# Kernel tuning notes

Measured on AMD Instinct MI355X. Metric: run time of the kernel, lower is better.

The kernel has to match this reference:

```python
import jax, jax.numpy as jnp
import numpy as np

NUM_NODES = 1024
INPUT_DIM = 64
HID_DIM = 64
MAX_DIFFUSION_STEP = 2
NUM_SUPPORTS = 2
OUT_DIM = 128
INPUT_SIZE = INPUT_DIM + HID_DIM          # F = 128
NUM_MATRICES = NUM_SUPPORTS * MAX_DIFFUSION_STEP + 1  # M = 5
BATCH = 64


def setup_inputs() -> dict:
    key = jax.random.key(0)
    k1, k2, k3, k4 = jax.random.split(key, 4)
    # scale supports like a normalized random-walk matrix so diffusion stays bounded
    supports = jax.random.normal(k1, (NUM_SUPPORTS, NUM_NODES, NUM_NODES), jnp.float32) / np.float32(np.sqrt(NUM_NODES))
    inputs = jax.random.normal(k2, (BATCH, NUM_NODES * INPUT_DIM), jnp.float32)
    state = jax.random.normal(k3, (BATCH, NUM_NODES * HID_DIM), jnp.float32)
    weight = jax.random.normal(k4, (INPUT_SIZE * NUM_MATRICES, OUT_DIM), jnp.float32) * 0.05
    biases = jnp.zeros((OUT_DIM,), jnp.float32)
    return {"supports": supports, "inputs": inputs, "state": state,
            "weight": weight, "biases": biases, "output_size": OUT_DIM}


def reference(supports, inputs, state, weight, biases, output_size):
    B = inputs.shape[0]
    x_in = inputs.reshape(B, NUM_NODES, -1)   # [B, N, input_dim]
    st = state.reshape(B, NUM_NODES, -1)      # [B, N, hid_dim]
    x0 = jnp.concatenate([x_in, st], axis=2)  # [B, N, F]

    xs = [x0]
    # Chebyshev-style diffusion: x_k = 2*A@x_{k-1} - x_{k-2}, per support
    for s in range(NUM_SUPPORTS):
        A = supports[s]
        x1 = jnp.einsum('nm,bmf->bnf', A, x0)
        xs.append(x1)
        xp2, xp1 = x0, x1
        for _ in range(2, MAX_DIFFUSION_STEP + 1):
            x2 = 2.0 * jnp.einsum('nm,bmf->bnf', A, xp1) - xp2
            xs.append(x2)
            xp2, xp1 = xp1, x2

    # torch does stack on dim1 -> [B,M,N,F], transpose to [B,N,F,M], reshape to F*M.
    # stacking on the last axis gives [B,N,F,M] directly (same memory order f*M+m).
    x = jnp.stack(xs, axis=3)                               # [B, N, F, M]
    x = x.reshape(B * NUM_NODES, INPUT_SIZE * NUM_MATRICES)  # [B*N, F*M]
    out = x @ weight + biases                                # [B*N, output_size]
    return out.reshape(B, NUM_NODES * output_size)
```

## Files before the change

### kernel.cpp

```cpp
#include <hip/hip_runtime.h>
#include <hip/hip_bf16.h>


typedef short bf16x8  __attribute__((ext_vector_type(8)));
typedef short short4v __attribute__((ext_vector_type(4)));
typedef float f32x4   __attribute__((ext_vector_type(4)));

constexpr size_t MB1    = 1024ull * 1024ull;
constexpr size_t SZ_MAT = 8192ull * 1024ull;
constexpr size_t OFF_PSTK = 0;
constexpr size_t OFF_SUPT = 4 * MB1;
constexpr size_t OFF_X0T  = 6 * MB1;
constexpr size_t OFF_X0NF = OFF_X0T  + SZ_MAT;
constexpr size_t OFF_XNF  = OFF_X0NF + SZ_MAT;
constexpr size_t OFF_W2T  = OFF_XNF  + 4 * SZ_MAT;

__device__ __forceinline__ unsigned short f2bf(float x) {
  union { float f; unsigned int u; } v; v.f = x;
  unsigned int r = v.u + 0x7fffu + ((v.u >> 16) & 1u);
  return (unsigned short)(r >> 16);
}

#define GLD16(gp, lp)                                                         \
  __builtin_amdgcn_global_load_lds(                                           \
      (const __attribute__((address_space(1))) unsigned int*)(gp),            \
      (__attribute__((address_space(3))) unsigned int*)(lp), 16, 0, 0)


__global__ __launch_bounds__(256)
void prep_kernel(const float* __restrict__ sup,
                 const float* __restrict__ weight,
                 const float* __restrict__ inputs,
                 const float* __restrict__ state,
                 unsigned short* __restrict__ ws) {
  __shared__ unsigned short tile[64][65];
  int bid = blockIdx.x;
  int tl  = threadIdx.x;

  if (bid < 2048) {
    size_t t = (size_t)bid * 256 + tl;
    const float4* src = (const float4*)sup;
    float4 v = src[t];
    size_t e = t * 4;
    size_t s = e >> 20;
    size_t r = e & (MB1 - 1);
    short4v o; o[0] = (short)f2bf(v.x); o[1] = (short)f2bf(v.y);
    o[2] = (short)f2bf(v.z); o[3] = (short)f2bf(v.w);
    *(short4v*)&ws[OFF_PSTK + 2 * s * MB1 + r] = o;
  } else if (bid < 2560) {
    int i = bid - 2048;
    int nt = i & 15, mt = (i >> 4) & 15, s = i >> 8;
    const float* A = sup + (size_t)s * MB1;
    unsigned short* AT = ws + OFF_SUPT + (size_t)s * MB1;
    int cl = tl & 63, rg = tl >> 6;
#pragma unroll 4
    for (int rr = 0; rr < 16; ++rr) {
      int rl = rr * 4 + rg;
      tile[rl][cl] = f2bf(A[(size_t)(nt * 64 + rl) * 1024 + mt * 64 + cl]);
    }
    __syncthreads();
#pragma unroll 4
    for (int rr = 0; rr < 16; ++rr) {
      int ml = rr * 4 + rg;
      AT[(size_t)(mt * 64 + ml) * 1024 + nt * 64 + cl] = tile[cl][ml];
    }
  } else if (bid < 2880) {
    int t = (bid - 2560) * 256 + tl;
    int o = t / 640, k = t % 640;
    int m = k >> 7, f = k & 127;
    ws[OFF_W2T + t] = f2bf(weight[(f * 5 + m) * 128 + o]);
  } else {
    int i = bid - 2880;
    int b = i & 63, nt = (i >> 6) & 15, ft = i >> 10;
    const float* src = ft ? state : inputs;
    unsigned short* x0t  = ws + OFF_X0T;
    unsigned short* x0nf = ws + OFF_X0NF;
    int fl = tl & 63, nr = tl >> 6;
#pragma unroll 4
    for (int rr = 0; rr < 16; ++rr) {
      int n_loc = rr * 4 + nr;
      float v = src[(size_t)b * 65536 + (size_t)(nt * 64 + n_loc) * 64 + fl];
      unsigned short bv = f2bf(v);
      tile[n_loc][fl] = bv;
      x0nf[(size_t)(nt * 64 + n_loc) * 8192 + b * 128 + ft * 64 + fl] = bv;
    }
    __syncthreads();
#pragma unroll 4
    for (int rr = 0; rr < 16; ++rr) {
      int f_loc = rr * 4 + nr;
      x0t[(size_t)(b * 128 + ft * 64 + f_loc) * 1024 + nt * 64 + fl] =
          tile[fl][f_loc];
    }
  }
}


__global__ __launch_bounds__(256, 2)
void mega_kernel(unsigned short* __restrict__ ws,
                 const float* __restrict__ bias,
                 float* __restrict__ dout) {
  extern __shared__ unsigned short lds[];

  const unsigned short* X0T = ws + OFF_X0T;
  const unsigned short* X0N = ws + OFF_X0NF;
  const unsigned short* W2  = ws + OFF_W2T;

  const int tid = threadIdx.x;
  const int l   = tid & 63;
  const int w   = tid >> 6;
  const int wr  = w >> 1, wc = w & 1;
  const int lm  = l & 15, q = l >> 4;

  int bid = blockIdx.x;
  int xcd = bid & 7, idx = bid >> 3;
  const int bm = xcd * 8 + (idx & 7);
  const int bn = idx >> 3;

  const int subrow = l >> 3;
  const int koff   = (((l & 7) << 3) ^ (subrow << 3));

  auto stage_x0t = [&](int kt) {
#pragma unroll
    for (int c = 0; c < 4; ++c) {
      int chunk = w * 4 + c, rowl = chunk * 8 + subrow;
      const unsigned short* gp =
          X0T + (size_t)(bm * 128 + rowl) * 1024 + kt * 64 + koff;
      GLD16(gp, &lds[chunk * 512]);
    }
  };
  auto stage_P = [&](int band, int kt) {
#pragma unroll
    for (int c = 0; c < 4; ++c) {
      int chunk = w * 4 + c, rowl = chunk * 8 + subrow;
      const unsigned short* gp = ws + OFF_PSTK + (size_t)band * MB1 +
                                 (size_t)(bn * 128 + rowl) * 1024 + kt * 64 + koff;
      GLD16(gp, &lds[8192 + chunk * 512]);
    }
  };
  auto stage_w2 = [&](int m, int kt2) {
#pragma unroll
    for (int c = 0; c < 4; ++c) {
      int chunk = w * 4 + c, rowl = chunk * 8 + subrow;
      const unsigned short* gp =
          W2 + (size_t)rowl * 640 + m * 128 + kt2 * 64 + koff;
      GLD16(gp, &lds[chunk * 512]);
    }
  };
  auto stage_x0n = [&](int kt2) {
#pragma unroll
    for (int c = 0; c < 4; ++c) {
      int chunk = w * 4 + c, rowl = chunk * 8 + subrow;
      const unsigned short* gp =
          X0N + (size_t)(bn * 128 + rowl) * 8192 + bm * 128 + kt2 * 64 + koff;
      GLD16(gp, &lds[8192 + chunk * 512]);
    }
  };

  f32x4 oacc[4][4] = {};

  for (int band = 0; band < 4; ++band) {
    f32x4 yacc[4][4] = {};
    for (int kt = 0; kt < 16; ++kt) {
      stage_x0t(kt);
      stage_P(band, kt);
      __syncthreads();
#pragma unroll
      for (int kk = 0; kk < 2; ++kk) {
        bf16x8 af[4], bfv[4];
#pragma unroll
        for (int i = 0; i < 4; ++i) {
          int row = wr * 64 + i * 16 + lm;
          int off = row * 64 + ((kk * 32 + (q << 3)) ^ ((row & 7) << 3));
          af[i] = *(const bf16x8*)&lds[off];
        }
#pragma unroll
        for (int j = 0; j < 4; ++j) {
          int row = wc * 64 + j * 16 + lm;
          int off = 8192 + row * 64 + ((kk * 32 + (q << 3)) ^ ((row & 7) << 3));
          bfv[j] = *(const bf16x8*)&lds[off];
        }
#pragma unroll
        for (int i = 0; i < 4; ++i)
#pragma unroll
          for (int j = 0; j < 4; ++j)
            yacc[i][j] = __builtin_amdgcn_mfma_f32_16x16x32_bf16(
                af[i], bfv[j], yacc[i][j], 0, 0, 0);
      }
      __syncthreads();
    }

#pragma unroll
    for (int i = 0; i < 4; ++i) {
      int f0 = wr * 64 + i * 16 + q * 4;
#pragma unroll
      for (int j = 0; j < 4; ++j) {
        int n = wc * 64 + j * 16 + lm;
        short4v pk;
#pragma unroll
        for (int r = 0; r < 4; ++r) pk[r] = (short)f2bf(yacc[i][j][r]);
        *(short4v*)&lds[16384 + n * 128 + (((f0 >> 3) ^ (n & 7)) << 3) +
                        (f0 & 7)] = pk;
      }
    }
    __syncthreads();

#pragma unroll
    for (int kt2 = 0; kt2 < 2; ++kt2) {
      stage_w2(band + 1, kt2);
      __syncthreads();
#pragma unroll
      for (int kk = 0; kk < 2; ++kk) {
        bf16x8 af[4], bfv[4];
#pragma unroll
        for (int i = 0; i < 4; ++i) {
          int row = wr * 64 + i * 16 + lm;
          int off = row * 64 + ((kk * 32 + (q << 3)) ^ ((row & 7) << 3));
          af[i] = *(const bf16x8*)&lds[off];
        }
#pragma unroll
        for (int j = 0; j < 4; ++j) {
          int n = wc * 64 + j * 16 + lm;
          int g = kt2 * 8 + kk * 4 + q;
          bfv[j] = *(const bf16x8*)&lds[16384 + n * 128 + ((g ^ (n & 7)) << 3)];
        }
#pragma unroll
        for (int i = 0; i < 4; ++i)
#pragma unroll
          for (int j = 0; j < 4; ++j)
            oacc[i][j] = __builtin_amdgcn_mfma_f32_16x16x32_bf16(
                af[i], bfv[j], oacc[i][j], 0, 0, 0);
      }
      __syncthreads();
    }
  }

#pragma unroll
  for (int kt2 = 0; kt2 < 2; ++kt2) {
    stage_w2(0, kt2);
    stage_x0n(kt2);
    __syncthreads();
#pragma unroll
    for (int kk = 0; kk < 2; ++kk) {
      bf16x8 af[4], bfv[4];
#pragma unroll
      for (int i = 0; i < 4; ++i) {
        int row = wr * 64 + i * 16 + lm;
        int off = row * 64 + ((kk * 32 + (q << 3)) ^ ((row & 7) << 3));
        af[i] = *(const bf16x8*)&lds[off];
      }
#pragma unroll
      for (int j = 0; j < 4; ++j) {
        int row = wc * 64 + j * 16 + lm;
        int off = 8192 + row * 64 + ((kk * 32 + (q << 3)) ^ ((row & 7) << 3));
        bfv[j] = *(const bf16x8*)&lds[off];
      }
#pragma unroll
      for (int i = 0; i < 4; ++i)
#pragma unroll
        for (int j = 0; j < 4; ++j)
          oacc[i][j] = __builtin_amdgcn_mfma_f32_16x16x32_bf16(
              af[i], bfv[j], oacc[i][j], 0, 0, 0);
    }
    __syncthreads();
  }

#pragma unroll
  for (int i = 0; i < 4; ++i) {
    int o0 = wr * 64 + i * 16 + q * 4;
    float4 bv = *(const float4*)&bias[o0];
#pragma unroll
    for (int j = 0; j < 4; ++j) {
      int n = bn * 128 + wc * 64 + j * 16 + lm;
      float4 v;
      v.x = oacc[i][j][0] + bv.x;
      v.y = oacc[i][j][1] + bv.y;
      v.z = oacc[i][j][2] + bv.z;
      v.w = oacc[i][j][3] + bv.w;
      *(float4*)&dout[(size_t)bm * 131072 + (size_t)n * 128 + o0] = v;
    }
  }
}


__global__ __launch_bounds__(256)
void psq_kernel(unsigned short* __restrict__ ws) {
  __shared__ short At[128 * 64];
  __shared__ short Bt[32 * 64];

  const int tid = threadIdx.x;
  const int l   = tid & 63;
  const int w   = tid >> 6;
  const int wr  = w >> 1, wc = w & 1;

  const int bm = blockIdx.x, bn = blockIdx.y, s = blockIdx.z;
  const unsigned short* A = ws + OFF_PSTK + (size_t)(2 * s) * MB1;
  const unsigned short* B = ws + OFF_SUPT + (size_t)s * MB1;

  const int subrow = l >> 3;
  const int koff   = (((l & 7) << 3) ^ (subrow << 3));

  f32x4 acc[4][1] = {};

  for (int kt = 0; kt < 16; ++kt) {
#pragma unroll
    for (int c = 0; c < 4; ++c) {
      int chunk = w * 4 + c, rowl = chunk * 8 + subrow;
      GLD16(A + (size_t)(bm * 128 + rowl) * 1024 + kt * 64 + koff,
            &At[chunk * 512]);
    }
    {
      int chunk = w, rowl = chunk * 8 + subrow;
      GLD16(B + (size_t)(bn * 32 + rowl) * 1024 + kt * 64 + koff,
            &Bt[chunk * 512]);
    }
    __syncthreads();

#pragma unroll
    for (int kk = 0; kk < 2; ++kk) {
      bf16x8 af[4], bfv;
#pragma unroll
      for (int i = 0; i < 4; ++i) {
        int row = wr * 64 + i * 16 + (l & 15);
        int off = row * 64 + ((kk * 32 + ((l >> 4) << 3)) ^ ((row & 7) << 3));
        af[i] = *(const bf16x8*)&At[off];
      }
      {
        int row = wc * 16 + (l & 15);
        int off = row * 64 + ((kk * 32 + ((l >> 4) << 3)) ^ ((row & 7) << 3));
        bfv = *(const bf16x8*)&Bt[off];
      }
#pragma unroll
      for (int i = 0; i < 4; ++i)
        acc[i][0] = __builtin_amdgcn_mfma_f32_16x16x32_bf16(af[i], bfv,
                                                            acc[i][0], 0, 0, 0);
    }
    __syncthreads();
  }

  unsigned short* P = ws + OFF_PSTK + (size_t)(2 * s + 1) * MB1;
#pragma unroll
  for (int i = 0; i < 4; ++i) {
    int rg0 = bm * 128 + wr * 64 + i * 16 + ((l >> 4) << 2);
    int cg  = bn * 32 + wc * 16 + (l & 15);
#pragma unroll
    for (int r = 0; r < 4; ++r) {
      int rg = rg0 + r;
      float v = 2.0f * acc[i][0][r] - (rg == cg ? 1.0f : 0.0f);
      P[(size_t)rg * 1024 + cg] = f2bf(v);
    }
  }
}


extern "C" void kernel_launch(void* const* d_in, const int* in_sizes, int n_in,
                              void* d_out, int out_size, void* d_ws, size_t ws_size,
                              hipStream_t stream) {
  (void)in_sizes; (void)n_in; (void)out_size; (void)ws_size;
  const float* supports = (const float*)d_in[0];
  const float* inputs   = (const float*)d_in[1];
  const float* state    = (const float*)d_in[2];
  const float* weight   = (const float*)d_in[3];
  const float* bias     = (const float*)d_in[4];
  float* out = (float*)d_out;
  unsigned short* ws = (unsigned short*)d_ws;

  prep_kernel<<<4928, 256, 0, stream>>>(supports, weight, inputs, state, ws);
  psq_kernel<<<dim3(8, 32, 2), 256, 0, stream>>>(ws);
  mega_kernel<<<512, 256, 65536, stream>>>(ws, bias, out);
}
```

Baseline: 113.7 us.

## Process two diffusion bands per K-loop to reuse X0T tiles across bands

The first GEMM now accumulates two P bands at once, with two P tiles staged in LDS per k-step. Each X0T tile is therefore loaded and read from LDS once for two bands, which halves the passes over X0T. The second GEMM now works in halves: only the half of the warps whose rows match writes its Y slice into a smaller LDS region before each W2 half-step. The cost is twice the yacc accumulator registers (a second 4x4 block per thread), a larger LDS footprint, and extra barriers.

Result: slower. 124.1 us (+9.2%).

```diff
diff --git a/kernel.cpp b/kernel.cpp
--- a/kernel.cpp
+++ b/kernel.cpp
@@ -128,21 +128,21 @@
       GLD16(gp, &lds[chunk * 512]);
     }
   };
-  auto stage_P = [&](int band, int kt) {
+  auto stage_P = [&](int band, int kt, int slot) {
 #pragma unroll
     for (int c = 0; c < 4; ++c) {
       int chunk = w * 4 + c, rowl = chunk * 8 + subrow;
       const unsigned short* gp = ws + OFF_PSTK + (size_t)band * MB1 +
                                  (size_t)(bn * 128 + rowl) * 1024 + kt * 64 + koff;
-      GLD16(gp, &lds[8192 + chunk * 512]);
+      GLD16(gp, &lds[8192 + slot * 8192 + chunk * 512]);
     }
   };
-  auto stage_w2 = [&](int m, int kt2) {
+  auto stage_w2 = [&](int m, int h) {
 #pragma unroll
     for (int c = 0; c < 4; ++c) {
       int chunk = w * 4 + c, rowl = chunk * 8 + subrow;
       const unsigned short* gp =
-          W2 + (size_t)rowl * 640 + m * 128 + kt2 * 64 + koff;
+          W2 + (size_t)rowl * 640 + m * 128 + h * 64 + koff;
       GLD16(gp, &lds[chunk * 512]);
     }
   };
@@ -158,15 +158,16 @@
 
   f32x4 oacc[4][4] = {};
 
-  for (int band = 0; band < 4; ++band) {
-    f32x4 yacc[4][4] = {};
+  for (int s = 0; s < 2; ++s) {
+    f32x4 yacc[2][4][4] = {};
     for (int kt = 0; kt < 16; ++kt) {
       stage_x0t(kt);
-      stage_P(band, kt);
+      stage_P(2 * s + 0, kt, 0);
+      stage_P(2 * s + 1, kt, 1);
       __syncthreads();
 #pragma unroll
       for (int kk = 0; kk < 2; ++kk) {
-        bf16x8 af[4], bfv[4];
+        bf16x8 af[4];
 #pragma unroll
         for (int i = 0; i < 4; ++i) {
           int row = wr * 64 + i * 16 + lm;
@@ -174,63 +175,69 @@
           af[i] = *(const bf16x8*)&lds[off];
         }
 #pragma unroll
-        for (int j = 0; j < 4; ++j) {
-          int row = wc * 64 + j * 16 + lm;
-          int off = 8192 + row * 64 + ((kk * 32 + (q << 3)) ^ ((row & 7) << 3));
-          bfv[j] = *(const bf16x8*)&lds[off];
+        for (int p = 0; p < 2; ++p) {
+#pragma unroll
+          for (int j = 0; j < 4; ++j) {
+            int row = wc * 64 + j * 16 + lm;
+            int off = 8192 + p * 8192 + row * 64 +
+                      ((kk * 32 + (q << 3)) ^ ((row & 7) << 3));
+            bf16x8 bfv = *(const bf16x8*)&lds[off];
+#pragma unroll
+            for (int i = 0; i < 4; ++i)
+              yacc[p][i][j] = __builtin_amdgcn_mfma_f32_16x16x32_bf16(
+                  af[i], bfv, yacc[p][i][j], 0, 0, 0);
+          }
         }
-#pragma unroll
-        for (int i = 0; i < 4; ++i)
-#pragma unroll
-          for (int j = 0; j < 4; ++j)
-            yacc[i][j] = __builtin_amdgcn_mfma_f32_16x16x32_bf16(
-                af[i], bfv[j], yacc[i][j], 0, 0, 0);
       }
       __syncthreads();
     }
 
 #pragma unroll
-    for (int i = 0; i < 4; ++i) {
-      int f0 = wr * 64 + i * 16 + q * 4;
-#pragma unroll
-      for (int j = 0; j < 4; ++j) {
-        int n = wc * 64 + j * 16 + lm;
-        short4v pk;
-#pragma unroll
-        for (int r = 0; r < 4; ++r) pk[r] = (short)f2bf(yacc[i][j][r]);
-        *(short4v*)&lds[16384 + n * 128 + (((f0 >> 3) ^ (n & 7)) << 3) +
-                        (f0 & 7)] = pk;
-      }
-    }
-    __syncthreads();
-
-#pragma unroll
-    for (int kt2 = 0; kt2 < 2; ++kt2) {
-      stage_w2(band + 1, kt2);
-      __syncthreads();
-#pragma unroll
-      for (int kk = 0; kk < 2; ++kk) {
-        bf16x8 af[4], bfv[4];
-#pragma unroll
-        for (int i = 0; i < 4; ++i) {
-          int row = wr * 64 + i * 16 + lm;
-          int off = row * 64 + ((kk * 32 + (q << 3)) ^ ((row & 7) << 3));
-          af[i] = *(const bf16x8*)&lds[off];
+    for (int p = 0; p < 2; ++p) {
+      int band = 2 * s + p;
+#pragma unroll
+      for (int h = 0; h < 2; ++h) {
+        stage_w2(band + 1, h);
+        if (wr == h) {
+#pragma unroll
+          for (int i = 0; i < 4; ++i) {
+            int fh0 = i * 16 + q * 4;
+#pragma unroll
+            for (int j = 0; j < 4; ++j) {
+              int n = wc * 64 + j * 16 + lm;
+              short4v pk;
+#pragma unroll
+              for (int r = 0; r < 4; ++r) pk[r] = (short)f2bf(yacc[p][i][j][r]);
+              *(short4v*)&lds[24576 + n * 64 + ((((fh0 >> 3) ^ (n & 7))) << 3) +
+                              (fh0 & 7)] = pk;
+            }
+          }
         }
-#pragma unroll
-        for (int j = 0; j < 4; ++j) {
-          int n = wc * 64 + j * 16 + lm;
-          int g = kt2 * 8 + kk * 4 + q;
-          bfv[j] = *(const bf16x8*)&lds[16384 + n * 128 + ((g ^ (n & 7)) << 3)];
+        __syncthreads();
+#pragma unroll
+        for (int kk = 0; kk < 2; ++kk) {
+          bf16x8 af[4], bfv[4];
+#pragma unroll
+          for (int i = 0; i < 4; ++i) {
+            int row = wr * 64 + i * 16 + lm;
+            int off = row * 64 + ((kk * 32 + (q << 3)) ^ ((row & 7) << 3));
+            af[i] = *(const bf16x8*)&lds[off];
+          }
+#pragma unroll
+          for (int j = 0; j < 4; ++j) {
+            int n = wc * 64 + j * 16 + lm;
+            int g = kk * 4 + q;
+            bfv[j] = *(const bf16x8*)&lds[24576 + n * 64 + ((g ^ (n & 7)) << 3)];
+          }
+#pragma unroll
+          for (int i = 0; i < 4; ++i)
+#pragma unroll
+            for (int j = 0; j < 4; ++j)
+              oacc[i][j] = __builtin_amdgcn_mfma_f32_16x16x32_bf16(
+                  af[i], bfv[j], oacc[i][j], 0, 0, 0);
         }
-#pragma unroll
-        for (int i = 0; i < 4; ++i)
-#pragma unroll
-          for (int j = 0; j < 4; ++j)
-            oacc[i][j] = __builtin_amdgcn_mfma_f32_16x16x32_bf16(
-                af[i], bfv[j], oacc[i][j], 0, 0, 0);
-      }
-      __syncthreads();
+        __syncthreads();
+      }
     }
   }
 
```
